# Performance work log

Hardware: AMD Instinct MI355X
Metric: run time of the kernel (lower is better)

Reference implementation:

```python
import jax, jax.numpy as jnp
import numpy as np

N, E, F_IN, H, OUT = 50000, 1600000, 128, 128, 32
NEG_SLOPE = 0.2


def setup_inputs() -> dict:
    key = jax.random.key(0)
    ks = jax.random.split(key, 9)
    s = lambda fan: 1.0 / np.sqrt(fan)
    x = jax.random.normal(ks[0], (N, F_IN), jnp.float32)
    edge_index = jax.random.randint(ks[1], (2, E), 0, N, jnp.int64)
    Wl1 = jax.random.normal(ks[2], (F_IN, H), jnp.float32) * s(F_IN)
    Wr1 = jax.random.normal(ks[3], (F_IN, H), jnp.float32) * s(F_IN)
    att1 = jax.random.normal(ks[4], (H,), jnp.float32) * s(H)
    b1 = jnp.zeros((H,), jnp.float32)
    Wl2 = jax.random.normal(ks[5], (H, OUT), jnp.float32) * s(H)
    Wr2 = jax.random.normal(ks[6], (H, OUT), jnp.float32) * s(H)
    att2 = jax.random.normal(ks[7], (OUT,), jnp.float32) * s(OUT)
    b2 = jnp.zeros((OUT,), jnp.float32)
    return {"x": x, "edge_index": edge_index, "Wl1": Wl1, "Wr1": Wr1,
            "att1": att1, "b1": b1, "Wl2": Wl2, "Wr2": Wr2, "att2": att2, "b2": b2}


def gatv2_layer(x, Wl, Wr, att, bias, src, dst, num_nodes):
    # PyG GATv2Conv (heads=1, concat=True, add_self_loops handled by caller)
    xl = x @ Wl  # source-side transform  [N, C]
    xr = x @ Wr  # target-side transform  [N, C]
    e = jax.nn.leaky_relu(xl[src] + xr[dst], NEG_SLOPE)  # [E, C]
    logits = e @ att  # [E]
    # segment softmax over incoming edges of each destination node
    m = jax.ops.segment_max(logits, dst, num_segments=num_nodes)  # [N]
    expv = jnp.exp(logits - m[dst])
    denom = jax.ops.segment_sum(expv, dst, num_segments=num_nodes)  # [N]
    alpha = expv / (denom[dst] + 1e-16)  # [E]
    out = jax.ops.segment_sum(xl[src] * alpha[:, None], dst, num_segments=num_nodes)
    return out + bias


def reference(x, edge_index, Wl1, Wr1, att1, b1, Wl2, Wr2, att2, b2):
    # add self-loops (PyG add_self_loops=True default)
    loops = jnp.arange(N, dtype=edge_index.dtype)
    src = jnp.concatenate([edge_index[0], loops])
    dst = jnp.concatenate([edge_index[1], loops])
    h = gatv2_layer(x, Wl1, Wr1, att1, b1, src, dst, N)
    h = jax.nn.relu(h)
    h = gatv2_layer(h, Wl2, Wr2, att2, b2, src, dst, N)
    return jax.nn.relu(h)
```

## Files before the change

kernel.cpp:

```cpp
#include <hip/hip_runtime.h>
#include <hip/hip_bf16.h>

#define N_NODES 50000
#define E_EDGES 1600000
#define E_TOT   (E_EDGES + N_NODES)
#define NEG_SLOPE 0.2f

#define NB       196
#define S1_TILE  2048
#define NT       ((E_TOT + S1_TILE - 1) / S1_TILE)
#define S2_CAP   12288

typedef _Float16 h2 __attribute__((ext_vector_type(2)));
typedef _Float16 h4 __attribute__((ext_vector_type(4)));
typedef _Float16 h8 __attribute__((ext_vector_type(8)));

__device__ __forceinline__ float fdot2h(h2 a, h2 b, float c)
{
#if __has_builtin(__builtin_amdgcn_fdot2)
    return __builtin_amdgcn_fdot2(a, b, c, false);
#else
    return c + (float)a[0] * (float)b[0] + (float)a[1] * (float)b[1];
#endif
}

__device__ __forceinline__ h2 habs2(h2 e)
{
    unsigned int u = __builtin_bit_cast(unsigned int, e) & 0x7FFF7FFFu;
    return __builtin_bit_cast(h2, u);
}

__global__ __launch_bounds__(256) void transform1_gemm(
    const float* __restrict__ x,
    const float* __restrict__ Wl, const float* __restrict__ Wr,
    _Float16* __restrict__ xl, _Float16* __restrict__ xr)
{
    __shared__ h2 xs2[16][128];
    __shared__ h2 ws2[16][128];
    const int n0 = blockIdx.x * 128;
    const float* __restrict__ W = blockIdx.y ? Wr : Wl;
    _Float16* __restrict__ Y = blockIdx.y ? xr : xl;
    const int t = threadIdx.x;
    const int tc = t & 15;
    const int tn = t >> 4;

    float acc[2][4][2][4];
#pragma unroll
    for (int nh = 0; nh < 2; ++nh)
#pragma unroll
        for (int i = 0; i < 4; ++i)
#pragma unroll
            for (int ch = 0; ch < 2; ++ch)
#pragma unroll
                for (int j = 0; j < 4; ++j) acc[nh][i][ch][j] = 0.f;

    for (int k0 = 0; k0 < 128; k0 += 32) {
        {
            const int node = t >> 1;
            const int kh = (t & 1) * 16;
            const int gn = n0 + node;
#pragma unroll
            for (int q = 0; q < 4; ++q) {
                float4 v = make_float4(0.f, 0.f, 0.f, 0.f);
                if (gn < N_NODES)
                    v = *(const float4*)&x[(size_t)gn * 128 + k0 + kh + q * 4];
                h2 p0 = {(_Float16)v.x, (_Float16)v.y};
                h2 p1 = {(_Float16)v.z, (_Float16)v.w};
                xs2[kh / 2 + q * 2 + 0][node] = p0;
                xs2[kh / 2 + q * 2 + 1][node] = p1;
            }
        }
        {
            const int c = t & 127;
            const int kq = (t >> 7) * 16;
#pragma unroll
            for (int ii = 0; ii < 8; ++ii) {
                h2 pw = {(_Float16)W[(size_t)(k0 + kq + 2 * ii) * 128 + c],
                         (_Float16)W[(size_t)(k0 + kq + 2 * ii + 1) * 128 + c]};
                ws2[kq / 2 + ii][c] = pw;
            }
        }
        __syncthreads();
#pragma unroll 4
        for (int k2 = 0; k2 < 16; ++k2) {
            h2 a0[4], a1[4], b0[4], b1[4];
#pragma unroll
            for (int j = 0; j < 4; ++j) {
                a0[j] = xs2[k2][tn * 4 + j];
                a1[j] = xs2[k2][64 + tn * 4 + j];
                b0[j] = ws2[k2][tc * 4 + j];
                b1[j] = ws2[k2][64 + tc * 4 + j];
            }
#pragma unroll
            for (int i = 0; i < 4; ++i)
#pragma unroll
                for (int j = 0; j < 4; ++j) {
                    acc[0][i][0][j] = fdot2h(a0[i], b0[j], acc[0][i][0][j]);
                    acc[0][i][1][j] = fdot2h(a0[i], b1[j], acc[0][i][1][j]);
                    acc[1][i][0][j] = fdot2h(a1[i], b0[j], acc[1][i][0][j]);
                    acc[1][i][1][j] = fdot2h(a1[i], b1[j], acc[1][i][1][j]);
                }
        }
        __syncthreads();
    }
#pragma unroll
    for (int nh = 0; nh < 2; ++nh)
#pragma unroll
        for (int i = 0; i < 4; ++i) {
            const int node = n0 + nh * 64 + tn * 4 + i;
            if (node < N_NODES) {
#pragma unroll
                for (int ch = 0; ch < 2; ++ch) {
                    h4 v;
                    v[0] = (_Float16)acc[nh][i][ch][0];
                    v[1] = (_Float16)acc[nh][i][ch][1];
                    v[2] = (_Float16)acc[nh][i][ch][2];
                    v[3] = (_Float16)acc[nh][i][ch][3];
                    *(h4*)&Y[(size_t)node * 128 + ch * 64 + tc * 4] = v;
                }
            }
        }
}

__global__ __launch_bounds__(256) void transform2_gemm(
    const _Float16* __restrict__ h,
    const float* __restrict__ Wl, const float* __restrict__ Wr,
    _Float16* __restrict__ hl, _Float16* __restrict__ hr)
{
    __shared__ h2 xs2[16][128];
    __shared__ h2 ws2[16][64];
    const int n0 = blockIdx.x * 128;
    const int t = threadIdx.x;
    const int tc = t & 15;
    const int tn = t >> 4;

    float acc[2][4][4];
#pragma unroll
    for (int nh = 0; nh < 2; ++nh)
#pragma unroll
        for (int i = 0; i < 4; ++i)
#pragma unroll
            for (int j = 0; j < 4; ++j) acc[nh][i][j] = 0.f;

    for (int k0 = 0; k0 < 128; k0 += 32) {
        {
            const int node = t >> 1;
            const int kh = (t & 1) * 16;
            const int gn = n0 + node;
            h8 v0 = {}, v1 = {};
            if (gn < N_NODES) {
                v0 = *(const h8*)&h[(size_t)gn * 128 + k0 + kh];
                v1 = *(const h8*)&h[(size_t)gn * 128 + k0 + kh + 8];
            }
#pragma unroll
            for (int q = 0; q < 4; ++q) {
                h2 p0 = {v0[2 * q], v0[2 * q + 1]};
                h2 p1 = {v1[2 * q], v1[2 * q + 1]};
                xs2[kh / 2 + q][node] = p0;
                xs2[kh / 2 + 4 + q][node] = p1;
            }
        }
        {
            const int c = t & 63;
            const int kq = (t >> 6) * 8;
            const float* __restrict__ Wm = (c < 32) ? Wl : Wr;
            const int wc = c & 31;
#pragma unroll
            for (int ii = 0; ii < 4; ++ii) {
                h2 pw = {(_Float16)Wm[(size_t)(k0 + kq + 2 * ii) * 32 + wc],
                         (_Float16)Wm[(size_t)(k0 + kq + 2 * ii + 1) * 32 + wc]};
                ws2[kq / 2 + ii][c] = pw;
            }
        }
        __syncthreads();
#pragma unroll 4
        for (int k2 = 0; k2 < 16; ++k2) {
            h2 a0[4], a1[4], b[4];
#pragma unroll
            for (int j = 0; j < 4; ++j) {
                a0[j] = xs2[k2][tn * 4 + j];
                a1[j] = xs2[k2][64 + tn * 4 + j];
                b[j] = ws2[k2][tc * 4 + j];
            }
#pragma unroll
            for (int i = 0; i < 4; ++i)
#pragma unroll
                for (int j = 0; j < 4; ++j) {
                    acc[0][i][j] = fdot2h(a0[i], b[j], acc[0][i][j]);
                    acc[1][i][j] = fdot2h(a1[i], b[j], acc[1][i][j]);
                }
        }
        __syncthreads();
    }
    _Float16* __restrict__ Y = (tc < 8) ? hl : hr;
    const int col = (tc < 8) ? tc * 4 : tc * 4 - 32;
#pragma unroll
    for (int nh = 0; nh < 2; ++nh)
#pragma unroll
        for (int i = 0; i < 4; ++i) {
            const int node = n0 + nh * 64 + tn * 4 + i;
            if (node < N_NODES) {
                h4 v;
                v[0] = (_Float16)acc[nh][i][0];
                v[1] = (_Float16)acc[nh][i][1];
                v[2] = (_Float16)acc[nh][i][2];
                v[3] = (_Float16)acc[nh][i][3];
                *(h4*)&Y[(size_t)node * 32 + col] = v;
            }
        }
}

__global__ __launch_bounds__(256) void tile_hist(
    const int* __restrict__ src, const int* __restrict__ dst,
    int* __restrict__ counts)
{
    __shared__ int hh[NB];
    const int t = threadIdx.x;
    const int base = blockIdx.x * S1_TILE;
    for (int i = t; i < NB; i += 256) hh[i] = 0;
    __syncthreads();
#pragma unroll
    for (int k = 0; k < S1_TILE / 256; ++k) {
        const int i = base + k * 256 + t;
        if (i < E_TOT) {
            const int d = (i < E_EDGES) ? dst[i] : (i - E_EDGES);
            atomicAdd(&hh[d >> 8], 1);
        }
    }
    __syncthreads();
    for (int b = t; b < NB; b += 256)
        counts[blockIdx.x * NB + b] = hh[b];
}

__global__ __launch_bounds__(1024) void row_scan(
    const int* __restrict__ counts, int* __restrict__ rstart,
    int* __restrict__ bcount)
{
    __shared__ int tmp[1024];
    const int b = blockIdx.x;
    const int t = threadIdx.x;
    const int v = (t < NT) ? counts[t * NB + b] : 0;
    tmp[t] = v;
    __syncthreads();
    for (int off = 1; off < 1024; off <<= 1) {
        int add = (t >= off) ? tmp[t - off] : 0;
        __syncthreads();
        tmp[t] += add;
        __syncthreads();
    }
    if (t < NT) rstart[b * NT + t] = tmp[t] - v;
    if (t == 1023) bcount[b] = tmp[1023];
}

__global__ __launch_bounds__(256) void bucket_base(
    const int* __restrict__ bcount, int* __restrict__ bbase)
{
    __shared__ int tmp[256];
    const int t = threadIdx.x;
    int v = (t < NB) ? bcount[t] : 0;
    tmp[t] = v;
    __syncthreads();
    for (int off = 1; off < 256; off <<= 1) {
        int add = (t >= off) ? tmp[t - off] : 0;
        __syncthreads();
        tmp[t] += add;
        __syncthreads();
    }
    if (t < NB) bbase[t] = tmp[t] - v;
    if (t == NB - 1) bbase[NB] = tmp[t];
}

__global__ __launch_bounds__(256) void tile_scatter(
    const int* __restrict__ src, const int* __restrict__ dst,
    const int* __restrict__ rstart, const int* __restrict__ bbase,
    unsigned int* __restrict__ bucket_data)
{
    __shared__ int hh[256];
    __shared__ int ls[256];
    __shared__ int cur[NB];
    __shared__ int rs[NB];
    __shared__ unsigned int srt[S1_TILE];
    const int t = threadIdx.x;
    const int tile = blockIdx.x;
    const int base = tile * S1_TILE;
    const int tcount = min(S1_TILE, E_TOT - base);

    hh[t] = 0;
    __syncthreads();

    int eb[S1_TILE / 256];
    unsigned int ee[S1_TILE / 256];
#pragma unroll
    for (int k = 0; k < S1_TILE / 256; ++k) {
        const int i = base + k * 256 + t;
        eb[k] = -1;
        if (i < E_TOT) {
            int s, d;
            if (i < E_EDGES) { s = src[i]; d = dst[i]; }
            else { s = i - E_EDGES; d = s; }
            const int b = d >> 8;
            eb[k] = b;
            ee[k] = ((unsigned)b << 24) | ((unsigned)(d & 255) << 16) | (unsigned)s;
            atomicAdd(&hh[b], 1);
        }
    }
    __syncthreads();
    {
        const int v = hh[t];
        ls[t] = v;
        __syncthreads();
        for (int off = 1; off < 256; off <<= 1) {
            int add = (t >= off) ? ls[t - off] : 0;
            __syncthreads();
            ls[t] += add;
            __syncthreads();
        }
        const int excl = ls[t] - v;
        if (t < NB) {
            cur[t] = excl;
            rs[t] = bbase[t] + rstart[t * NT + tile] - excl;
        }
    }
    __syncthreads();
#pragma unroll
    for (int k = 0; k < S1_TILE / 256; ++k) {
        if (eb[k] >= 0) {
            const int pos = atomicAdd(&cur[eb[k]], 1);
            srt[pos] = ee[k];
        }
    }
    __syncthreads();
    for (int i = t; i < tcount; i += 256) {
        const unsigned int e = srt[i];
        bucket_data[rs[e >> 24] + i] = e;
    }
}

__global__ __launch_bounds__(1024) void bucket_sort(
    const unsigned int* __restrict__ bucket_data,
    const int* __restrict__ bbase,
    int* __restrict__ offs, unsigned short* __restrict__ sorted_src)
{
    __shared__ int hist[256];
    __shared__ int cur[256];
    __shared__ int tmp[256];
    __shared__ unsigned short srt[S2_CAP];
    const int b = blockIdx.x;
    const int t = threadIdx.x;
    const int lo = bbase[b], hi = bbase[b + 1];
    const int c = hi - lo;
    if (t < 256) hist[t] = 0;
    __syncthreads();
    for (int i = t; i < c; i += 1024)
        atomicAdd(&hist[(bucket_data[lo + i] >> 16) & 255u], 1);
    __syncthreads();
    if (t < 256) tmp[t] = hist[t];
    __syncthreads();
    for (int off = 1; off < 256; off <<= 1) {
        int add = (t < 256 && t >= off) ? tmp[t - off] : 0;
        __syncthreads();
        if (t < 256) tmp[t] += add;
        __syncthreads();
    }
    if (t < 256) {
        const int excl = tmp[t] - hist[t];
        cur[t] = excl;
        const int node = b * 256 + t;
        if (node < N_NODES) offs[node] = lo + excl;
    }
    if (b == 0 && t == 0) offs[N_NODES] = E_TOT;
    __syncthreads();
    for (int i = t; i < c; i += 1024) {
        const unsigned int e = bucket_data[lo + i];
        const int pos = atomicAdd(&cur[(e >> 16) & 255u], 1);
        srt[pos] = (unsigned short)(e & 0xFFFFu);
    }
    __syncthreads();
    for (int i = t; i < c; i += 1024)
        sorted_src[lo + i] = srt[i];
}

template <int C, int LPG, typename OUT_T>
__global__ __launch_bounds__(256) void gat_edge_pass(
    const _Float16* __restrict__ xl, const _Float16* __restrict__ xr,
    const float* __restrict__ att, const float* __restrict__ bias,
    const int* __restrict__ offs, const unsigned short* __restrict__ ssrc,
    OUT_T* __restrict__ out)
{
    constexpr int GPB = 256 / LPG;
    static_assert(C == LPG * 8, "8 halves per lane");
    const int node = blockIdx.x * GPB + threadIdx.x / LPG;
    if (node >= N_NODES) return;
    const int lane = threadIdx.x % LPG;
    const int cb = lane * 8;

    h2 a6[4], a4[4], r2[4];
    {
        const h8 rv = *(const h8*)(xr + (size_t)node * C + cb);
#pragma unroll
        for (int i = 0; i < 4; ++i) {
            const float av0 = att[cb + 2 * i], av1 = att[cb + 2 * i + 1];
            h2 t6 = {(_Float16)(0.6f * av0), (_Float16)(0.6f * av1)};
            h2 t4 = {(_Float16)(0.4f * av0), (_Float16)(0.4f * av1)};
            a6[i] = t6; a4[i] = t4;
            h2 rr = {rv[2 * i], rv[2 * i + 1]};
            r2[i] = rr;
        }
    }
    float acc[8];
#pragma unroll
    for (int v = 0; v < 8; ++v) acc[v] = 0.f;
    float m = -3.0e38f, denom = 0.f;

    const int p1 = offs[node + 1];
    int p = offs[node];

    for (; p + 4 <= p1; p += 4) {
        const int s0 = ssrc[p], s1 = ssrc[p + 1];
        const int s2 = ssrc[p + 2], s3 = ssrc[p + 3];
        const h8 x0 = *(const h8*)(xl + (size_t)s0 * C + cb);
        const h8 x1 = *(const h8*)(xl + (size_t)s1 * C + cb);
        const h8 x2 = *(const h8*)(xl + (size_t)s2 * C + cb);
        const h8 x3 = *(const h8*)(xl + (size_t)s3 * C + cb);
        float d0 = 0.f, d1 = 0.f, d2 = 0.f, d3 = 0.f;
#pragma unroll
        for (int i = 0; i < 4; ++i) {
            h2 xa = {x0[2 * i], x0[2 * i + 1]};
            h2 xb = {x1[2 * i], x1[2 * i + 1]};
            h2 xc = {x2[2 * i], x2[2 * i + 1]};
            h2 xd = {x3[2 * i], x3[2 * i + 1]};
            h2 e0 = xa + r2[i], e1 = xb + r2[i];
            h2 e2 = xc + r2[i], e3 = xd + r2[i];
            d0 = fdot2h(a6[i], e0, fdot2h(a4[i], habs2(e0), d0));
            d1 = fdot2h(a6[i], e1, fdot2h(a4[i], habs2(e1), d1));
            d2 = fdot2h(a6[i], e2, fdot2h(a4[i], habs2(e2), d2));
            d3 = fdot2h(a6[i], e3, fdot2h(a4[i], habs2(e3), d3));
        }
#pragma unroll
        for (int off = LPG >> 1; off; off >>= 1) {
            d0 += __shfl_xor(d0, off);
            d1 += __shfl_xor(d1, off);
            d2 += __shfl_xor(d2, off);
            d3 += __shfl_xor(d3, off);
        }
        const float pm = fmaxf(fmaxf(d0, d1), fmaxf(d2, d3));
        if (__builtin_expect(pm > m + 8.f, 0)) {
            const float sc = __expf(m - pm);
            m = pm;
            denom *= sc;
#pragma unroll
            for (int v = 0; v < 8; ++v) acc[v] *= sc;
        }
        const float w0 = __expf(d0 - m), w1 = __expf(d1 - m);
        const float w2 = __expf(d2 - m), w3 = __expf(d3 - m);
        denom += (w0 + w1) + (w2 + w3);
        const h2 wA = {(_Float16)w0, (_Float16)w1};
        const h2 wB = {(_Float16)w2, (_Float16)w3};
#pragma unroll
        for (int v = 0; v < 8; ++v) {
            h2 pA = {x0[v], x1[v]};
            h2 pB = {x2[v], x3[v]};
            acc[v] = fdot2h(wA, pA, fdot2h(wB, pB, acc[v]));
        }
    }
    for (; p + 2 <= p1; p += 2) {
        const int s0 = ssrc[p], s1 = ssrc[p + 1];
        const h8 x0 = *(const h8*)(xl + (size_t)s0 * C + cb);
        const h8 x1 = *(const h8*)(xl + (size_t)s1 * C + cb);
        float d0 = 0.f, d1 = 0.f;
#pragma unroll
        for (int i = 0; i < 4; ++i) {
            h2 xa = {x0[2 * i], x0[2 * i + 1]};
            h2 xb = {x1[2 * i], x1[2 * i + 1]};
            h2 e0 = xa + r2[i], e1 = xb + r2[i];
            d0 = fdot2h(a6[i], e0, fdot2h(a4[i], habs2(e0), d0));
            d1 = fdot2h(a6[i], e1, fdot2h(a4[i], habs2(e1), d1));
        }
#pragma unroll
        for (int off = LPG >> 1; off; off >>= 1) {
            d0 += __shfl_xor(d0, off);
            d1 += __shfl_xor(d1, off);
        }
        const float pm = fmaxf(d0, d1);
        if (__builtin_expect(pm > m + 8.f, 0)) {
            const float sc = __expf(m - pm);
            m = pm;
            denom *= sc;
#pragma unroll
            for (int v = 0; v < 8; ++v) acc[v] *= sc;
        }
        const float w0 = __expf(d0 - m), w1 = __expf(d1 - m);
        denom += w0 + w1;
        const h2 wA = {(_Float16)w0, (_Float16)w1};
#pragma unroll
        for (int v = 0; v < 8; ++v) {
            h2 pA = {x0[v], x1[v]};
            acc[v] = fdot2h(wA, pA, acc[v]);
        }
    }
    if (p < p1) {
        const int s0 = ssrc[p];
        const h8 x0 = *(const h8*)(xl + (size_t)s0 * C + cb);
        float d0 = 0.f;
#pragma unroll
        for (int i = 0; i < 4; ++i) {
            h2 xa = {x0[2 * i], x0[2 * i + 1]};
            h2 e0 = xa + r2[i];
            d0 = fdot2h(a6[i], e0, fdot2h(a4[i], habs2(e0), d0));
        }
#pragma unroll
        for (int off = LPG >> 1; off; off >>= 1) d0 += __shfl_xor(d0, off);
        if (d0 > m + 8.f) {
            const float sc = __expf(m - d0);
            m = d0;
            denom *= sc;
#pragma unroll
            for (int v = 0; v < 8; ++v) acc[v] *= sc;
        }
        const float w0 = __expf(d0 - m);
        denom += w0;
        const h2 wA = {(_Float16)w0, (_Float16)0.f};
#pragma unroll
        for (int v = 0; v < 8; ++v) {
            h2 pA = {x0[v], x0[v]};
            acc[v] = fdot2h(wA, pA, acc[v]);
        }
    }

    const float inv = 1.f / (denom + 1e-16f);
    if constexpr (sizeof(OUT_T) == 2) {
        h8 o;
#pragma unroll
        for (int v = 0; v < 8; ++v)
            o[v] = (_Float16)fmaxf(fmaf(acc[v], inv, bias[cb + v]), 0.f);
        *(h8*)&out[(size_t)node * C + cb] = o;
    } else {
        float4 o0, o1;
        o0.x = fmaxf(fmaf(acc[0], inv, bias[cb + 0]), 0.f);
        o0.y = fmaxf(fmaf(acc[1], inv, bias[cb + 1]), 0.f);
        o0.z = fmaxf(fmaf(acc[2], inv, bias[cb + 2]), 0.f);
        o0.w = fmaxf(fmaf(acc[3], inv, bias[cb + 3]), 0.f);
        o1.x = fmaxf(fmaf(acc[4], inv, bias[cb + 4]), 0.f);
        o1.y = fmaxf(fmaf(acc[5], inv, bias[cb + 5]), 0.f);
        o1.z = fmaxf(fmaf(acc[6], inv, bias[cb + 6]), 0.f);
        o1.w = fmaxf(fmaf(acc[7], inv, bias[cb + 7]), 0.f);
        *(float4*)&out[(size_t)node * C + cb] = o0;
        *(float4*)&out[(size_t)node * C + cb + 4] = o1;
    }
}

extern "C" void kernel_launch(void* const* d_in, const int* in_sizes, int n_in,
                              void* d_out, int out_size, void* d_ws, size_t ws_size,
                              hipStream_t stream)
{
    const float* x    = (const float*)d_in[0];
    const int*   ei   = (const int*)d_in[1];
    const float* Wl1  = (const float*)d_in[2];
    const float* Wr1  = (const float*)d_in[3];
    const float* att1 = (const float*)d_in[4];
    const float* b1   = (const float*)d_in[5];
    const float* Wl2  = (const float*)d_in[6];
    const float* Wr2  = (const float*)d_in[7];
    const float* att2 = (const float*)d_in[8];
    const float* b2   = (const float*)d_in[9];
    float* out = (float*)d_out;

    const int* e_src = ei;
    const int* e_dst = ei + E_EDGES;

    char* ws = (char*)d_ws;
    _Float16* xl = (_Float16*)(ws + 0);
    _Float16* xr = (_Float16*)(ws + 25600000);
    _Float16* h  = (_Float16*)(ws + 51200000);
    unsigned short* sorted_src = (unsigned short*)(ws + 76800000);
    int* offs   = (int*)(ws + 83400192);
    int* bbase  = (int*)(ws + 83600384);
    int* bcount = (int*)(ws + 83602432);
    unsigned int* bucket_data = (unsigned int*)(ws + 51200000);
    int* counts = (int*)(ws + 58000000);
    int* rstart = (int*)(ws + 58700000);
    _Float16* hl = xl;
    _Float16* hr = xr;

    transform1_gemm<<<dim3((N_NODES + 127) / 128, 2), 256, 0, stream>>>(
        x, Wl1, Wr1, xl, xr);

    tile_hist<<<NT, 256, 0, stream>>>(e_src, e_dst, counts);
    row_scan<<<NB, 1024, 0, stream>>>(counts, rstart, bcount);
    bucket_base<<<1, 256, 0, stream>>>(bcount, bbase);
    tile_scatter<<<NT, 256, 0, stream>>>(e_src, e_dst, rstart, bbase, bucket_data);
    bucket_sort<<<NB, 1024, 0, stream>>>(bucket_data, bbase, offs, sorted_src);

    gat_edge_pass<128, 16, _Float16><<<N_NODES * 16 / 256, 256, 0, stream>>>(
        xl, xr, att1, b1, offs, sorted_src, h);

    transform2_gemm<<<(N_NODES + 127) / 128, 256, 0, stream>>>(
        h, Wl2, Wr2, hl, hr);

    gat_edge_pass<32, 4, float><<<(N_NODES * 4 + 255) / 256, 256, 0, stream>>>(
        hl, hr, att2, b2, offs, sorted_src, out);
}
```

Before: 171.4 us.

## Prefetch gathered rows in edge pass, use wave-shuffle scans, enlarge sort tiles

```diff
diff --git a/kernel.cpp b/kernel.cpp
--- a/kernel.cpp
+++ b/kernel.cpp
@@ -7,7 +7,7 @@
 #define NEG_SLOPE 0.2f
 
 #define NB       196
-#define S1_TILE  2048
+#define S1_TILE  4096
 #define NT       ((E_TOT + S1_TILE - 1) / S1_TILE)
 #define S2_CAP   12288
 
@@ -28,6 +28,16 @@
 {
     unsigned int u = __builtin_bit_cast(unsigned int, e) & 0x7FFF7FFFu;
     return __builtin_bit_cast(h2, u);
+}
+
+__device__ __forceinline__ int wave_iscan(int v, int lane)
+{
+#pragma unroll
+    for (int off = 1; off < 64; off <<= 1) {
+        int u = __shfl_up(v, off);
+        if (lane >= off) v += u;
+    }
+    return v;
 }
 
 __global__ __launch_bounds__(256) void transform1_gemm(
@@ -210,89 +220,95 @@
         }
 }
 
-__global__ __launch_bounds__(256) void tile_hist(
+__global__ __launch_bounds__(512) void tile_hist(
     const int* __restrict__ src, const int* __restrict__ dst,
     int* __restrict__ counts)
 {
     __shared__ int hh[NB];
     const int t = threadIdx.x;
     const int base = blockIdx.x * S1_TILE;
-    for (int i = t; i < NB; i += 256) hh[i] = 0;
-    __syncthreads();
-#pragma unroll
-    for (int k = 0; k < S1_TILE / 256; ++k) {
-        const int i = base + k * 256 + t;
+    for (int i = t; i < NB; i += 512) hh[i] = 0;
+    __syncthreads();
+#pragma unroll
+    for (int k = 0; k < S1_TILE / 512; ++k) {
+        const int i = base + k * 512 + t;
         if (i < E_TOT) {
             const int d = (i < E_EDGES) ? dst[i] : (i - E_EDGES);
             atomicAdd(&hh[d >> 8], 1);
         }
     }
     __syncthreads();
-    for (int b = t; b < NB; b += 256)
+    for (int b = t; b < NB; b += 512)
         counts[blockIdx.x * NB + b] = hh[b];
 }
 
-__global__ __launch_bounds__(1024) void row_scan(
+__global__ __launch_bounds__(512) void row_scan(
     const int* __restrict__ counts, int* __restrict__ rstart,
     int* __restrict__ bcount)
 {
-    __shared__ int tmp[1024];
+    __shared__ int wsum[8];
     const int b = blockIdx.x;
     const int t = threadIdx.x;
+    const int lane = t & 63, wid = t >> 6;
     const int v = (t < NT) ? counts[t * NB + b] : 0;
-    tmp[t] = v;
-    __syncthreads();
-    for (int off = 1; off < 1024; off <<= 1) {
-        int add = (t >= off) ? tmp[t - off] : 0;
-        __syncthreads();
-        tmp[t] += add;
-        __syncthreads();
-    }
-    if (t < NT) rstart[b * NT + t] = tmp[t] - v;
-    if (t == 1023) bcount[b] = tmp[1023];
+    int inc = wave_iscan(v, lane);
+    if (lane == 63) wsum[wid] = inc;
+    __syncthreads();
+    if (t == 0) {
+        int s = 0;
+#pragma unroll
+        for (int w = 0; w < 8; ++w) { int u = wsum[w]; wsum[w] = s; s += u; }
+    }
+    __syncthreads();
+    const int excl = inc - v + wsum[wid];
+    if (t < NT) rstart[b * NT + t] = excl;
+    if (t == 511) bcount[b] = excl;
 }
 
 __global__ __launch_bounds__(256) void bucket_base(
     const int* __restrict__ bcount, int* __restrict__ bbase)
 {
-    __shared__ int tmp[256];
+    __shared__ int wsum[4];
     const int t = threadIdx.x;
+    const int lane = t & 63, wid = t >> 6;
     int v = (t < NB) ? bcount[t] : 0;
-    tmp[t] = v;
-    __syncthreads();
-    for (int off = 1; off < 256; off <<= 1) {
-        int add = (t >= off) ? tmp[t - off] : 0;
-        __syncthreads();
-        tmp[t] += add;
-        __syncthreads();
-    }
-    if (t < NB) bbase[t] = tmp[t] - v;
-    if (t == NB - 1) bbase[NB] = tmp[t];
-}
-
-__global__ __launch_bounds__(256) void tile_scatter(
+    int inc = wave_iscan(v, lane);
+    if (lane == 63) wsum[wid] = inc;
+    __syncthreads();
+    if (t == 0) {
+        int s = 0;
+#pragma unroll
+        for (int w = 0; w < 4; ++w) { int u = wsum[w]; wsum[w] = s; s += u; }
+    }
+    __syncthreads();
+    const int excl = inc - v + wsum[wid];
+    if (t < NB) bbase[t] = excl;
+    if (t == NB - 1) bbase[NB] = excl + v;
+}
+
+__global__ __launch_bounds__(512) void tile_scatter(
     const int* __restrict__ src, const int* __restrict__ dst,
     const int* __restrict__ rstart, const int* __restrict__ bbase,
     unsigned int* __restrict__ bucket_data)
 {
     __shared__ int hh[256];
-    __shared__ int ls[256];
     __shared__ int cur[NB];
     __shared__ int rs[NB];
+    __shared__ int wsum[8];
     __shared__ unsigned int srt[S1_TILE];
     const int t = threadIdx.x;
     const int tile = blockIdx.x;
     const int base = tile * S1_TILE;
     const int tcount = min(S1_TILE, E_TOT - base);
 
-    hh[t] = 0;
-    __syncthreads();
-
-    int eb[S1_TILE / 256];
-    unsigned int ee[S1_TILE / 256];
-#pragma unroll
-    for (int k = 0; k < S1_TILE / 256; ++k) {
-        const int i = base + k * 256 + t;
+    for (int i = t; i < 256; i += 512) hh[i] = 0;
+    __syncthreads();
+
+    int eb[S1_TILE / 512];
+    unsigned int ee[S1_TILE / 512];
+#pragma unroll
+    for (int k = 0; k < S1_TILE / 512; ++k) {
+        const int i = base + k * 512 + t;
         eb[k] = -1;
         if (i < E_TOT) {
             int s, d;
@@ -306,31 +322,33 @@
     }
     __syncthreads();
     {
-        const int v = hh[t];
-        ls[t] = v;
-        __syncthreads();
-        for (int off = 1; off < 256; off <<= 1) {
-            int add = (t >= off) ? ls[t - off] : 0;
-            __syncthreads();
-            ls[t] += add;
-            __syncthreads();
-        }
-        const int excl = ls[t] - v;
+        const int lane = t & 63, wid = t >> 6;
+        const int v = (t < 256) ? hh[t] : 0;
+        int inc = wave_iscan(v, lane);
+        if (lane == 63 && wid < 4) wsum[wid] = inc;
+        __syncthreads();
+        if (t == 0) {
+            int s = 0;
+#pragma unroll
+            for (int w = 0; w < 4; ++w) { int u = wsum[w]; wsum[w] = s; s += u; }
+        }
+        __syncthreads();
         if (t < NB) {
+            const int excl = inc - v + wsum[wid];
             cur[t] = excl;
             rs[t] = bbase[t] + rstart[t * NT + tile] - excl;
         }
     }
     __syncthreads();
 #pragma unroll
-    for (int k = 0; k < S1_TILE / 256; ++k) {
+    for (int k = 0; k < S1_TILE / 512; ++k) {
         if (eb[k] >= 0) {
             const int pos = atomicAdd(&cur[eb[k]], 1);
             srt[pos] = ee[k];
         }
     }
     __syncthreads();
-    for (int i = t; i < tcount; i += 256) {
+    for (int i = t; i < tcount; i += 512) {
         const unsigned int e = srt[i];
         bucket_data[rs[e >> 24] + i] = e;
     }
@@ -343,7 +361,7 @@
 {
     __shared__ int hist[256];
     __shared__ int cur[256];
-    __shared__ int tmp[256];
+    __shared__ int wsum[4];
     __shared__ unsigned short srt[S2_CAP];
     const int b = blockIdx.x;
     const int t = threadIdx.x;
@@ -354,19 +372,24 @@
     for (int i = t; i < c; i += 1024)
         atomicAdd(&hist[(bucket_data[lo + i] >> 16) & 255u], 1);
     __syncthreads();
-    if (t < 256) tmp[t] = hist[t];
-    __syncthreads();
-    for (int off = 1; off < 256; off <<= 1) {
-        int add = (t < 256 && t >= off) ? tmp[t - off] : 0;
-        __syncthreads();
-        if (t < 256) tmp[t] += add;
-        __syncthreads();
-    }
-    if (t < 256) {
-        const int excl = tmp[t] - hist[t];
-        cur[t] = excl;
-        const int node = b * 256 + t;
-        if (node < N_NODES) offs[node] = lo + excl;
+    {
+        const int lane = t & 63, wid = t >> 6;
+        const int v = (t < 256) ? hist[t] : 0;
+        int inc = wave_iscan(v, lane);
+        if (lane == 63 && wid < 4) wsum[wid] = inc;
+        __syncthreads();
+        if (t == 0) {
+            int s = 0;
+#pragma unroll
+            for (int w = 0; w < 4; ++w) { int u = wsum[w]; wsum[w] = s; s += u; }
+        }
+        __syncthreads();
+        if (t < 256) {
+            const int excl = inc - v + wsum[wid];
+            cur[t] = excl;
+            const int node = b * 256 + t;
+            if (node < N_NODES) offs[node] = lo + excl;
+        }
     }
     if (b == 0 && t == 0) offs[N_NODES] = E_TOT;
     __syncthreads();
@@ -412,16 +435,41 @@
     for (int v = 0; v < 8; ++v) acc[v] = 0.f;
     float m = -3.0e38f, denom = 0.f;
 
+    const int pB = offs[node];
     const int p1 = offs[node + 1];
-    int p = offs[node];
-
-    for (; p + 4 <= p1; p += 4) {
+    int p = pB;
+    const int nq = (p1 - pB) >> 2;
+
+    h8 x0, x1, x2, x3;
+    int i0 = 0, i1 = 0, i2 = 0, i3 = 0;
+    if (nq > 0) {
         const int s0 = ssrc[p], s1 = ssrc[p + 1];
         const int s2 = ssrc[p + 2], s3 = ssrc[p + 3];
-        const h8 x0 = *(const h8*)(xl + (size_t)s0 * C + cb);
-        const h8 x1 = *(const h8*)(xl + (size_t)s1 * C + cb);
-        const h8 x2 = *(const h8*)(xl + (size_t)s2 * C + cb);
-        const h8 x3 = *(const h8*)(xl + (size_t)s3 * C + cb);
+        x0 = *(const h8*)(xl + (size_t)s0 * C + cb);
+        x1 = *(const h8*)(xl + (size_t)s1 * C + cb);
+        x2 = *(const h8*)(xl + (size_t)s2 * C + cb);
+        x3 = *(const h8*)(xl + (size_t)s3 * C + cb);
+    }
+    if (nq > 1) {
+        i0 = ssrc[p + 4]; i1 = ssrc[p + 5];
+        i2 = ssrc[p + 6]; i3 = ssrc[p + 7];
+    }
+
+    for (int q = 0; q < nq; ++q) {
+        const bool more  = (q + 1 < nq);
+        const bool more2 = (q + 2 < nq);
+        int j0 = 0, j1 = 0, j2 = 0, j3 = 0;
+        if (more2) {
+            j0 = ssrc[p + 8];  j1 = ssrc[p + 9];
+            j2 = ssrc[p + 10]; j3 = ssrc[p + 11];
+        }
+        h8 y0 = {}, y1 = {}, y2 = {}, y3 = {};
+        if (more) {
+            y0 = *(const h8*)(xl + (size_t)i0 * C + cb);
+            y1 = *(const h8*)(xl + (size_t)i1 * C + cb);
+            y2 = *(const h8*)(xl + (size_t)i2 * C + cb);
+            y3 = *(const h8*)(xl + (size_t)i3 * C + cb);
+        }
         float d0 = 0.f, d1 = 0.f, d2 = 0.f, d3 = 0.f;
 #pragma unroll
         for (int i = 0; i < 4; ++i) {
@@ -462,49 +510,17 @@
             h2 pB = {x2[v], x3[v]};
             acc[v] = fdot2h(wA, pA, fdot2h(wB, pB, acc[v]));
         }
-    }
-    for (; p + 2 <= p1; p += 2) {
-        const int s0 = ssrc[p], s1 = ssrc[p + 1];
-        const h8 x0 = *(const h8*)(xl + (size_t)s0 * C + cb);
-        const h8 x1 = *(const h8*)(xl + (size_t)s1 * C + cb);
-        float d0 = 0.f, d1 = 0.f;
+        if (more)  { x0 = y0; x1 = y1; x2 = y2; x3 = y3; }
+        if (more2) { i0 = j0; i1 = j1; i2 = j2; i3 = j3; }
+        p += 4;
+    }
+    for (; p < p1; ++p) {
+        const int s0 = ssrc[p];
+        const h8 t0 = *(const h8*)(xl + (size_t)s0 * C + cb);
+        float d0 = 0.f;
 #pragma unroll
         for (int i = 0; i < 4; ++i) {
-            h2 xa = {x0[2 * i], x0[2 * i + 1]};
-            h2 xb = {x1[2 * i], x1[2 * i + 1]};
-            h2 e0 = xa + r2[i], e1 = xb + r2[i];
-            d0 = fdot2h(a6[i], e0, fdot2h(a4[i], habs2(e0), d0));
-            d1 = fdot2h(a6[i], e1, fdot2h(a4[i], habs2(e1), d1));
-        }
-#pragma unroll
-        for (int off = LPG >> 1; off; off >>= 1) {
-            d0 += __shfl_xor(d0, off);
-            d1 += __shfl_xor(d1, off);
-        }
-        const float pm = fmaxf(d0, d1);
-        if (__builtin_expect(pm > m + 8.f, 0)) {
-            const float sc = __expf(m - pm);
-            m = pm;
-            denom *= sc;
-#pragma unroll
-            for (int v = 0; v < 8; ++v) acc[v] *= sc;
-        }
-        const float w0 = __expf(d0 - m), w1 = __expf(d1 - m);
-        denom += w0 + w1;
-        const h2 wA = {(_Float16)w0, (_Float16)w1};
-#pragma unroll
-        for (int v = 0; v < 8; ++v) {
-            h2 pA = {x0[v], x1[v]};
-            acc[v] = fdot2h(wA, pA, acc[v]);
-        }
-    }
-    if (p < p1) {
-        const int s0 = ssrc[p];
-        const h8 x0 = *(const h8*)(xl + (size_t)s0 * C + cb);
-        float d0 = 0.f;
-#pragma unroll
-        for (int i = 0; i < 4; ++i) {
-            h2 xa = {x0[2 * i], x0[2 * i + 1]};
+            h2 xa = {t0[2 * i], t0[2 * i + 1]};
             h2 e0 = xa + r2[i];
             d0 = fdot2h(a6[i], e0, fdot2h(a4[i], habs2(e0), d0));
         }
@@ -522,7 +538,7 @@
         const h2 wA = {(_Float16)w0, (_Float16)0.f};
 #pragma unroll
         for (int v = 0; v < 8; ++v) {
-            h2 pA = {x0[v], x0[v]};
+            h2 pA = {t0[v], t0[v]};
             acc[v] = fdot2h(wA, pA, acc[v]);
         }
     }
@@ -578,17 +594,17 @@
     int* bcount = (int*)(ws + 83602432);
     unsigned int* bucket_data = (unsigned int*)(ws + 51200000);
     int* counts = (int*)(ws + 58000000);
-    int* rstart = (int*)(ws + 58700000);
+    int* rstart = (int*)(ws + 58400000);
     _Float16* hl = xl;
     _Float16* hr = xr;
 
     transform1_gemm<<<dim3((N_NODES + 127) / 128, 2), 256, 0, stream>>>(
         x, Wl1, Wr1, xl, xr);
 
-    tile_hist<<<NT, 256, 0, stream>>>(e_src, e_dst, counts);
-    row_scan<<<NB, 1024, 0, stream>>>(counts, rstart, bcount);
+    tile_hist<<<NT, 512, 0, stream>>>(e_src, e_dst, counts);
+    row_scan<<<NB, 512, 0, stream>>>(counts, rstart, bcount);
     bucket_base<<<1, 256, 0, stream>>>(bcount, bbase);
-    tile_scatter<<<NT, 256, 0, stream>>>(e_src, e_dst, rstart, bbase, bucket_data);
+    tile_scatter<<<NT, 512, 0, stream>>>(e_src, e_dst, rstart, bbase, bucket_data);
     bucket_sort<<<NB, 1024, 0, stream>>>(bucket_data, bbase, offs, sorted_src);
 
     gat_edge_pass<128, 16, _Float16><<<N_NODES * 16 / 256, 256, 0, stream>>>(
```

After: 186.7 us. 8.9% more time.
